# Optimization experiments

Measured on AMD Instinct MI355X. Metric: run time of the kernel, lower is better.

The kernel has to match this reference:

```python
import jax, jax.numpy as jnp
import numpy as np

N_HEAD = 16
D_MODEL = 1024
D_HEAD = D_MODEL // N_HEAD
B, T = 2, 2048


def setup_inputs() -> dict:
    key = jax.random.key(0)
    k1, k2, k3 = jax.random.split(key, 3)
    x = jax.random.normal(k1, (B, T, D_MODEL), dtype=jnp.float32)
    w_attn = jax.random.normal(k2, (3 * D_MODEL, D_MODEL), dtype=jnp.float32) * (D_MODEL ** -0.5)
    w_proj = jax.random.normal(k3, (D_MODEL, D_MODEL), dtype=jnp.float32) * (D_MODEL ** -0.5)
    return {"x": x, "w_attn": w_attn, "w_proj": w_proj}


def _rms_norm(x):
    eps = jnp.asarray(jnp.finfo(x.dtype).eps, x.dtype)
    var = jnp.mean(jnp.square(x), axis=-1, keepdims=True)
    return x * jax.lax.rsqrt(var + eps)


def _rotate_half(x):
    x1, x2 = jnp.split(x, 2, axis=-1)
    return jnp.concatenate((-x2, x1), axis=-1)


def reference(x, w_attn, w_proj):
    Bx, Tx, C = x.shape
    qkv = jnp.einsum('btc,fc->btf', x, w_attn)  # [B,T,3C]
    q, k, v = jnp.split(qkv, 3, axis=-1)
    # [B, H, T, Dh]
    q = q.reshape(Bx, Tx, N_HEAD, D_HEAD).transpose(0, 2, 1, 3)
    k = k.reshape(Bx, Tx, N_HEAD, D_HEAD).transpose(0, 2, 1, 3)
    v = v.reshape(Bx, Tx, N_HEAD, D_HEAD).transpose(0, 2, 1, 3)
    # QK RMSNorm (no learned weight)
    q = _rms_norm(q)
    k = _rms_norm(k)
    # Rotary embedding over full d_head: freqs tiled twice
    inv_freq = 1.0 / (10000.0 ** (jnp.arange(0, D_HEAD, 2, dtype=jnp.float32) / D_HEAD))
    t = jnp.arange(Tx, dtype=jnp.float32)
    freqs = jnp.einsum('i,j->ij', t, inv_freq)  # [T, Dh/2]
    emb = jnp.concatenate((freqs, freqs), axis=-1)  # [T, Dh]
    cos = jnp.cos(emb)[None, None, :, :]
    sin = jnp.sin(emb)[None, None, :, :]
    q = q * cos + _rotate_half(q) * sin
    k = k * cos + _rotate_half(k) * sin
    # Causal SDPA
    scale = D_HEAD ** -0.5
    scores = jnp.einsum('bhqd,bhkd->bhqk', q, k) * scale
    causal = jnp.tril(jnp.ones((Tx, Tx), dtype=bool))
    scores = jnp.where(causal[None, None], scores, jnp.asarray(-jnp.inf, scores.dtype))
    attn = jax.nn.softmax(scores, axis=-1)
    y = jnp.einsum('bhqk,bhkd->bhqd', attn, v)
    y = y.transpose(0, 2, 1, 3).reshape(Bx, Tx, C)
    return jnp.einsum('btc,oc->bto', y, w_proj)
```

## Files before the change

kernel.cpp:

```cpp
#include <hip/hip_runtime.h>
#include <cstdint>
#include <cstddef>


typedef short bf16x8 __attribute__((ext_vector_type(8)));
typedef float floatx4 __attribute__((ext_vector_type(4)));
typedef float floatx2 __attribute__((ext_vector_type(2)));
typedef unsigned short ushortx8 __attribute__((ext_vector_type(8)));
typedef unsigned short ushortx4 __attribute__((ext_vector_type(4)));
typedef unsigned int uintx2 __attribute__((ext_vector_type(2)));

#define DEVI __device__ __forceinline__

DEVI float bf2f(unsigned short u) {
    unsigned int x = ((unsigned int)u) << 16;
    return __builtin_bit_cast(float, x);
}
DEVI unsigned short f2bf(float f) {
    unsigned int u = __builtin_bit_cast(unsigned int, f);
    u += 0x7fffu + ((u >> 16) & 1u);
    return (unsigned short)(u >> 16);
}
DEVI unsigned int pkbf2(float a, float b) {
    unsigned int ua = __builtin_bit_cast(unsigned int, a) + 0x8000u;
    unsigned int ub = __builtin_bit_cast(unsigned int, b) + 0x8000u;
    return __builtin_amdgcn_perm(ub, ua, 0x07060302);
}

DEVI void glds16(const unsigned short* g, unsigned short* l) {
    __builtin_amdgcn_global_load_lds(
        (const __attribute__((address_space(1))) unsigned int*)g,
        (__attribute__((address_space(3))) unsigned int*)l, 16, 0, 0);
}

DEVI void cast8(unsigned short* dst, const float* src) {
    floatx4 a = *(const floatx4*)src;
    floatx4 b = *(const floatx4*)(src + 4);
    ushortx8 o;
    o[0] = f2bf(a[0]); o[1] = f2bf(a[1]); o[2] = f2bf(a[2]); o[3] = f2bf(a[3]);
    o[4] = f2bf(b[0]); o[5] = f2bf(b[1]); o[6] = f2bf(b[2]); o[7] = f2bf(b[3]);
    *(ushortx8*)dst = o;
}

__global__ __launch_bounds__(256)
void cast_inputs(const float* __restrict__ x, const float* __restrict__ wa,
                 const float* __restrict__ wp,
                 unsigned short* __restrict__ xb, unsigned short* __restrict__ wab,
                 unsigned short* __restrict__ wpb, float* __restrict__ ropetab)
{
    size_t g = (size_t)blockIdx.x * 256 + threadIdx.x;
    size_t stride = (size_t)gridDim.x * 256;
    for (size_t i = g; i < (4194304 / 8); i += stride) cast8(xb  + i * 8, x  + i * 8);
    for (size_t i = g; i < (3145728 / 8); i += stride) cast8(wab + i * 8, wa + i * 8);
    for (size_t i = g; i < (1048576 / 8); i += stride) cast8(wpb + i * 8, wp + i * 8);
    for (size_t i = g; i < 65536; i += stride) {
        int t = (int)(i >> 5), f = (int)(i & 31);
        float ang = (float)t * __expf(-(float)f * 0.28782313662425572f);
        float sn, cs;
        __sincosf(ang, &sn, &cs);
        ropetab[2 * i]     = cs;
        ropetab[2 * i + 1] = sn;
    }
}

__global__ __launch_bounds__(512, 2)
void gemm_qkv_8ph(const unsigned short* __restrict__ A,
                  const unsigned short* __restrict__ B,
                  const float* __restrict__ ropetab,
                  unsigned short* __restrict__ Cqk,
                  unsigned short* __restrict__ Vt)
{
    __shared__ __align__(16) unsigned short lds[2][2][256 * 64];

    const int tid  = threadIdx.x;
    const int lane = tid & 63;
    const int w    = tid >> 6;
    const int wm   = w >> 2;
    const int wn   = w & 3;
    const int quad = lane >> 4;
    const int lm   = lane & 15;

    const int lin = blockIdx.y * 12 + blockIdx.x;
    const int s   = (lin & 7) * 24 + (lin >> 3);
    const int m0  = (s / 12) * 256;
    const int n0  = (s % 12) * 256;

    const int srow = tid >> 3;
    const int scol = (((tid & 7) ^ ((tid >> 3) & 7)) * 8);
    const int ldst = w * 512;

#define STG_A(u, WBi, kq) glds16(&A[(size_t)(m0 + (u) * 64 + srow) * 1024 + (kq) + scol], \
                                 &lds[WBi][0][(u) * 4096 + ldst])
#define STG_B(u, WBi, kq) glds16(&B[(size_t)(n0 + (u) * 64 + srow) * 1024 + (kq) + scol], \
                                 &lds[WBi][1][(u) * 4096 + ldst])
#define RD_A(RBi, rrow, kk) (*(const bf16x8*)&lds[RBi][0][(rrow) * 64 + ((((kk) * 4 + quad) ^ ((rrow) & 7)) * 8)])
#define RD_B(RBi, rrow, kk) (*(const bf16x8*)&lds[RBi][1][(rrow) * 64 + ((((kk) * 4 + quad) ^ ((rrow) & 7)) * 8)])

    floatx4 acc[8][4] = {};
    bf16x8 afr[4][2];
    bf16x8 bfr[4][2];

#define MQ(MB, JB)                                                              \
  do {                                                                          \
    _Pragma("unroll")                                                           \
    for (int kk = 0; kk < 2; ++kk)                                              \
      _Pragma("unroll")                                                         \
      for (int mi = 0; mi < 4; ++mi)                                            \
        _Pragma("unroll")                                                       \
        for (int j2 = 0; j2 < 2; ++j2)                                          \
          acc[(MB) + mi][(JB) + j2] = __builtin_amdgcn_mfma_f32_16x16x32_bf16(  \
              afr[mi][kk], bfr[(JB) + j2][kk], acc[(MB) + mi][(JB) + j2], 0, 0, 0); \
  } while (0)

#define TILE(RBi, WBi, KT, LASTF)                                               \
  do {                                                                          \
    const int kn = ((KT) + 1) * 64;                                             \
    if (!(LASTF)) { STG_B(0, WBi, kn); STG_B(1, WBi, kn); }                     \
    _Pragma("unroll")                                                           \
    for (int kk = 0; kk < 2; ++kk) {                                            \
      _Pragma("unroll")                                                         \
      for (int mi = 0; mi < 4; ++mi)                                            \
        afr[mi][kk] = RD_A(RBi, wm * 128 + mi * 16 + lm, kk);                   \
      _Pragma("unroll")                                                         \
      for (int j2 = 0; j2 < 2; ++j2)                                            \
        bfr[j2][kk] = RD_B(RBi, wn * 64 + j2 * 16 + lm, kk);                    \
    }                                                                           \
    asm volatile("s_waitcnt lgkmcnt(8)" ::: "memory");                          \
    __builtin_amdgcn_s_barrier();                                               \
    asm volatile("s_waitcnt lgkmcnt(0)" ::: "memory");                          \
    __builtin_amdgcn_s_setprio(1); MQ(0, 0); __builtin_amdgcn_s_setprio(0);     \
    __builtin_amdgcn_s_barrier();                                               \
    if (!(LASTF)) { STG_B(2, WBi, kn); STG_B(3, WBi, kn); }                     \
    _Pragma("unroll")                                                           \
    for (int kk = 0; kk < 2; ++kk)                                              \
      _Pragma("unroll")                                                         \
      for (int j2 = 0; j2 < 2; ++j2)                                            \
        bfr[2 + j2][kk] = RD_B(RBi, wn * 64 + (2 + j2) * 16 + lm, kk);          \
    if (!(LASTF)) { asm volatile("s_waitcnt vmcnt(4)" ::: "memory"); }          \
    else          { asm volatile("s_waitcnt vmcnt(0)" ::: "memory"); }          \
    __builtin_amdgcn_s_barrier();                                               \
    asm volatile("s_waitcnt lgkmcnt(0)" ::: "memory");                          \
    __builtin_amdgcn_s_setprio(1); MQ(0, 2); __builtin_amdgcn_s_setprio(0);     \
    __builtin_amdgcn_s_barrier();                                               \
    if (!(LASTF)) { STG_A(0, WBi, kn); STG_A(2, WBi, kn); }                     \
    _Pragma("unroll")                                                           \
    for (int kk = 0; kk < 2; ++kk)                                              \
      _Pragma("unroll")                                                         \
      for (int mi = 0; mi < 4; ++mi)                                            \
        afr[mi][kk] = RD_A(RBi, wm * 128 + 64 + mi * 16 + lm, kk);              \
    __builtin_amdgcn_s_barrier();                                               \
    asm volatile("s_waitcnt lgkmcnt(0)" ::: "memory");                          \
    __builtin_amdgcn_s_setprio(1); MQ(4, 2); __builtin_amdgcn_s_setprio(0);     \
    __builtin_amdgcn_s_barrier();                                               \
    if (!(LASTF)) { STG_A(1, WBi, kn); STG_A(3, WBi, kn);                       \
                    asm volatile("s_waitcnt vmcnt(2)" ::: "memory"); }          \
    __builtin_amdgcn_s_barrier();                                               \
    __builtin_amdgcn_s_setprio(1); MQ(4, 0); __builtin_amdgcn_s_setprio(0);     \
    __builtin_amdgcn_s_barrier();                                               \
  } while (0)

    STG_B(0, 0, 0); STG_B(1, 0, 0); STG_B(2, 0, 0); STG_B(3, 0, 0);
    STG_A(0, 0, 0); STG_A(2, 0, 0); STG_A(1, 0, 0); STG_A(3, 0, 0);
    asm volatile("s_waitcnt vmcnt(2)" ::: "memory");
    __builtin_amdgcn_s_barrier();

    for (int kt = 0; kt < 14; kt += 2) {
        TILE(0, 1, kt, false);
        TILE(1, 0, kt + 1, false);
    }
    TILE(0, 1, 14, false);
    TILE(1, 0, 15, true);

    const bool is_v = (n0 + wn * 64) >= 2048;
    if (!is_v) {
        const floatx2* rtab = (const floatx2*)ropetab;
        #pragma unroll
        for (int mi = 0; mi < 8; ++mi) {
            float rn[4];
            #pragma unroll
            for (int r = 0; r < 4; ++r) {
                float ss = 0.0f;
                #pragma unroll
                for (int j = 0; j < 4; ++j) ss += acc[mi][j][r] * acc[mi][j][r];
                ss += __shfl_xor(ss, 1, 64);
                ss += __shfl_xor(ss, 2, 64);
                ss += __shfl_xor(ss, 4, 64);
                ss += __shfl_xor(ss, 8, 64);
                rn[r] = rsqrtf(ss * (1.0f / 64.0f) + 1.1920929e-07f);
            }
            #pragma unroll
            for (int r = 0; r < 4; ++r) {
                int row = m0 + wm * 128 + mi * 16 + quad * 4 + r;
                int t = row & 2047;
                floatx2 cs0 = rtab[t * 32 + lm];
                floatx2 cs1 = rtab[t * 32 + 16 + lm];
                float g = rn[r];
                #pragma unroll
                for (int j = 0; j < 4; ++j) {
                    int d = j * 16 + lm;
                    float cs = (j & 1) ? cs1[0] : cs0[0];
                    float sn = (j & 1) ? cs1[1] : cs0[1];
                    float v  = acc[mi][j][r] * g;
                    float vp = acc[mi][j ^ 2][r] * g;
                    float sgn = (d < 32) ? -1.0f : 1.0f;
                    Cqk[(size_t)row * 2048 + (n0 + wn * 64 + d)] =
                        f2bf(v * cs + sgn * vp * sn);
                }
            }
        }
    } else {
        #pragma unroll
        for (int mi = 0; mi < 8; ++mi)
            #pragma unroll
            for (int j = 0; j < 4; ++j) {
                int col  = n0 + wn * 64 + j * 16 + lm;
                int row0 = m0 + wm * 128 + mi * 16 + quad * 4;
                int bq = row0 >> 11, t0 = row0 & 2047;
                ushortx4 pk;
                #pragma unroll
                for (int r = 0; r < 4; ++r) pk[r] = f2bf(acc[mi][j][r]);
                *(ushortx4*)&Vt[((size_t)(bq * 1024 + (col - 2048))) * 2048 + t0] = pk;
            }
    }
#undef TILE
#undef MQ
#undef RD_A
#undef RD_B
#undef STG_A
#undef STG_B
}

template <int BN, int BK>
__global__ __launch_bounds__(256)
void gemm_bt(const unsigned short* __restrict__ A, const unsigned short* __restrict__ B,
             float* __restrict__ Cf, int M, int N, int K)
{
    constexpr int WCOLS = (BN == 128) ? 2 : 1;
    constexpr int WROWS = 4 / WCOLS;
    constexpr int MI    = 128 / (16 * WROWS);
    constexpr int LPR   = BK / 8;
    constexpr int RPI   = 64 / LPR;

    __shared__ __align__(16) unsigned short As[128 * BK];
    __shared__ __align__(16) unsigned short Bs[BN * BK];

    const int tid  = threadIdx.x;
    const int lane = tid & 63;
    const int w    = tid >> 6;
    const int wm   = w / WCOLS, wn = w % WCOLS;
    const int quad = lane >> 4;
    const int lm   = lane & 15;
    const int m0 = blockIdx.y * 128;
    const int n0 = blockIdx.x * BN;
    const int sr = lane / LPR;
    const int sc = (lane % LPR) * 8;

    floatx4 acc[MI][4] = {};

    for (int k0 = 0; k0 < K; k0 += BK) {
        __syncthreads();
        #pragma unroll
        for (int i = 0; i < 32 / RPI; ++i) {
            int r = w * 32 + i * RPI;
            glds16(&A[(size_t)(m0 + r + sr) * K + k0 + sc], &As[r * BK]);
        }
        #pragma unroll
        for (int i = 0; i < (BN / 4) / RPI; ++i) {
            int r = w * (BN / 4) + i * RPI;
            glds16(&B[(size_t)(n0 + r + sr) * K + k0 + sc], &Bs[r * BK]);
        }
        __syncthreads();

        #pragma unroll
        for (int kk = 0; kk < BK / 32; ++kk) {
            bf16x8 a[MI];
            #pragma unroll
            for (int i = 0; i < MI; ++i)
                a[i] = *(const bf16x8*)&As[(wm * (16 * MI) + i * 16 + lm) * BK + kk * 32 + quad * 8];
            #pragma unroll
            for (int j = 0; j < 4; ++j) {
                bf16x8 b = *(const bf16x8*)&Bs[(wn * 64 + j * 16 + lm) * BK + kk * 32 + quad * 8];
                #pragma unroll
                for (int i = 0; i < MI; ++i)
                    acc[i][j] = __builtin_amdgcn_mfma_f32_16x16x32_bf16(a[i], b, acc[i][j], 0, 0, 0);
            }
        }
    }

    #pragma unroll
    for (int i = 0; i < MI; ++i)
        #pragma unroll
        for (int j = 0; j < 4; ++j) {
            int col  = n0 + wn * 64 + j * 16 + lm;
            int row0 = m0 + wm * (16 * MI) + i * 16 + quad * 4;
            #pragma unroll
            for (int r = 0; r < 4; ++r)
                Cf[(size_t)(row0 + r) * N + col] = acc[i][j][r];
        }
}

#define ATTN_EXP(SA, QROW, PROW, KT, DG)                                       \
  do {                                                                         \
    _Pragma("unroll")                                                          \
    for (int j = 0; j < 4; ++j) {                                              \
      float p0 = exp2f((SA)[j][0] * c1 - c2);                                  \
      float p1 = exp2f((SA)[j][1] * c1 - c2);                                  \
      float p2 = exp2f((SA)[j][2] * c1 - c2);                                  \
      float p3 = exp2f((SA)[j][3] * c1 - c2);                                  \
      if (DG) {                                                                \
        int kb = (KT) * 64 + j * 16 + quad * 4;                                \
        if (kb + 0 > (QROW)) p0 = 0.0f;                                        \
        if (kb + 1 > (QROW)) p1 = 0.0f;                                        \
        if (kb + 2 > (QROW)) p2 = 0.0f;                                        \
        if (kb + 3 > (QROW)) p3 = 0.0f;                                        \
      }                                                                        \
      uintx2 pk;                                                               \
      pk[0] = pkbf2(p0, p1);                                                   \
      pk[1] = pkbf2(p2, p3);                                                   \
      *(uintx2*)&QPs[(PROW) * 64 + (((2 * j + (quad >> 1)) ^ sx) * 8) + (quad & 1) * 4] = pk; \
    }                                                                          \
  } while (0)

#define ATTN_STEP(KSc, VSc, KSn, VSn, KT, DG, LAST)                            \
  do {                                                                         \
    if (!(LAST)) {                                                             \
      *(ushortx8*)&(KSn)[wkA] = kregA; *(ushortx8*)&(KSn)[wkB] = kregB;        \
      *(ushortx8*)&(VSn)[wkA] = vregA; *(ushortx8*)&(VSn)[wkB] = vregB;        \
      if ((KT) + 2 <= lastk) {                                                 \
        kregA = *(const ushortx8*)kpA; kregB = *(const ushortx8*)kpB;          \
        vregA = *(const ushortx8*)vpA; vregB = *(const ushortx8*)vpB;          \
        kpA += (size_t)64 * 2048; kpB += (size_t)64 * 2048;                    \
        vpA += 64; vpB += 64;                                                  \
      }                                                                        \
    }                                                                          \
    floatx4 sa0[4] = {}, sa1[4] = {};                                          \
    _Pragma("unroll")                                                          \
    for (int kk = 0; kk < 2; ++kk)                                             \
      _Pragma("unroll")                                                        \
      for (int j = 0; j < 4; ++j) {                                            \
        bf16x8 kf = *(const bf16x8*)&(KSc)[(j * 16 + lm) * 64 + (((kk * 4 + quad) ^ sx) * 8)]; \
        sa0[j] = __builtin_amdgcn_mfma_f32_16x16x32_bf16(kf, qf0[kk], sa0[j], 0, 0, 0); \
        sa1[j] = __builtin_amdgcn_mfma_f32_16x16x32_bf16(kf, qf1[kk], sa1[j], 0, 0, 0); \
      }                                                                        \
    ATTN_EXP(sa0, qrow0, w * 32 + lm,      KT, DG);                            \
    ATTN_EXP(sa1, qrow1, w * 32 + 16 + lm, KT, DG);                            \
    _Pragma("unroll")                                                          \
    for (int kk = 0; kk < 2; ++kk) {                                           \
      bf16x8 pf0 = *(const bf16x8*)&QPs[(w * 32 + lm) * 64 + (((kk * 4 + quad) ^ sx) * 8)]; \
      bf16x8 pf1 = *(const bf16x8*)&QPs[(w * 32 + 16 + lm) * 64 + (((kk * 4 + quad) ^ sx) * 8)]; \
      _Pragma("unroll")                                                        \
      for (int j = 0; j < 4; ++j) {                                            \
        bf16x8 vf = *(const bf16x8*)&(VSc)[(j * 16 + lm) * 64 + (((kk * 4 + quad) ^ sx) * 8)]; \
        o0[j] = __builtin_amdgcn_mfma_f32_16x16x32_bf16(pf0, vf, o0[j], 0, 0, 0); \
        o1[j] = __builtin_amdgcn_mfma_f32_16x16x32_bf16(pf1, vf, o1[j], 0, 0, 0); \
      }                                                                        \
      l0 = __builtin_amdgcn_mfma_f32_16x16x32_bf16(pf0, ones, l0, 0, 0, 0);    \
      l1 = __builtin_amdgcn_mfma_f32_16x16x32_bf16(pf1, ones, l1, 0, 0, 0);    \
    }                                                                          \
    if (!(LAST)) __syncthreads();                                              \
  } while (0)

__global__ __launch_bounds__(256, 3)
void attention(const unsigned short* __restrict__ qk,
               const unsigned short* __restrict__ Vt,
               unsigned short* __restrict__ Y)
{
    __shared__ __align__(16) unsigned short QPs[128 * 64];
    __shared__ __align__(16) unsigned short Ks0[64 * 64];
    __shared__ __align__(16) unsigned short Ks1[64 * 64];
    __shared__ __align__(16) unsigned short Vs0[64 * 64];
    __shared__ __align__(16) unsigned short Vs1[64 * 64];

    const int tid  = threadIdx.x;
    const int lane = tid & 63;
    const int w    = tid >> 6;
    const int quad = lane >> 4;
    const int lm   = lane & 15;
    const int sx   = lm & 7;

    const int bh = blockIdx.x;
    const int qt = 15 - blockIdx.y;
    const int b  = bh >> 4, h = bh & 15;
    const int q0 = qt * 128;
    const int qrow0 = q0 + w * 32 + lm;
    const int qrow1 = qrow0 + 16;
    const int lastk = 2 * qt + 1;

    const int sr  = tid >> 3;
    const int sch = tid & 7;
    const int swz = ((sch ^ (sr & 7)) * 8);
    const int wkA = sr * 64 + swz;
    const int wkB = (sr + 32) * 64 + swz;

    const unsigned short* kpA = qk + (size_t)b * 2048 * 2048 + 1024 + h * 64
                              + (size_t)sr * 2048 + sch * 8;
    const unsigned short* kpB = kpA + (size_t)32 * 2048;
    const unsigned short* vpA = Vt + (size_t)bh * 64 * 2048 + (size_t)sr * 2048 + sch * 8;
    const unsigned short* vpB = vpA + (size_t)32 * 2048;

    #pragma unroll
    for (int p = 0; p < 4; ++p) {
        int row = p * 32 + sr;
        *(ushortx8*)&QPs[row * 64 + swz] =
            *(const ushortx8*)&qk[((size_t)(b * 2048 + q0 + row)) * 2048 + h * 64 + sch * 8];
    }

    ushortx8 kregA = *(const ushortx8*)kpA, kregB = *(const ushortx8*)kpB;
    ushortx8 vregA = *(const ushortx8*)vpA, vregB = *(const ushortx8*)vpB;
    kpA += (size_t)64 * 2048; kpB += (size_t)64 * 2048; vpA += 64; vpB += 64;
    *(ushortx8*)&Ks0[wkA] = kregA; *(ushortx8*)&Ks0[wkB] = kregB;
    *(ushortx8*)&Vs0[wkA] = vregA; *(ushortx8*)&Vs0[wkB] = vregB;
    kregA = *(const ushortx8*)kpA; kregB = *(const ushortx8*)kpB;
    vregA = *(const ushortx8*)vpA; vregB = *(const ushortx8*)vpB;
    kpA += (size_t)64 * 2048; kpB += (size_t)64 * 2048; vpA += 64; vpB += 64;
    __syncthreads();

    bf16x8 qf0[2], qf1[2];
    #pragma unroll
    for (int kk = 0; kk < 2; ++kk) {
        qf0[kk] = *(const bf16x8*)&QPs[(w * 32 + lm) * 64 + (((kk * 4 + quad) ^ sx) * 8)];
        qf1[kk] = *(const bf16x8*)&QPs[(w * 32 + 16 + lm) * 64 + (((kk * 4 + quad) ^ sx) * 8)];
    }

    bf16x8 ones;
    #pragma unroll
    for (int i = 0; i < 8; ++i) ones[i] = (short)0x3F80;

    floatx4 o0[4] = {}, o1[4] = {};
    floatx4 l0 = {}, l1 = {};
    const float c1 = 0.125f * 1.44269504f;
    const float c2 = 8.0f   * 1.44269504f;

    int kt = 0;
    for (; kt + 3 < 2 * qt + 2; kt += 2) {
        ATTN_STEP(Ks0, Vs0, Ks1, Vs1, kt,     false, false);
        ATTN_STEP(Ks1, Vs1, Ks0, Vs0, kt + 1, false, false);
    }
    ATTN_STEP(Ks0, Vs0, Ks1, Vs1, kt,     true, false);
    ATTN_STEP(Ks1, Vs1, Ks0, Vs0, kt + 1, true, true);

    float rinv0[4], rinv1[4];
    #pragma unroll
    for (int r = 0; r < 4; ++r) { rinv0[r] = 1.0f / l0[r]; rinv1[r] = 1.0f / l1[r]; }

    #pragma unroll
    for (int j = 0; j < 4; ++j) {
        int colg = h * 64 + j * 16 + lm;
        #pragma unroll
        for (int r = 0; r < 4; ++r) {
            int rowg0 = q0 + w * 32 + quad * 4 + r;
            Y[((size_t)(b * 2048 + rowg0)) * 1024 + colg] = f2bf(o0[j][r] * rinv0[r]);
            Y[((size_t)(b * 2048 + rowg0 + 16)) * 1024 + colg] = f2bf(o1[j][r] * rinv1[r]);
        }
    }
}

extern "C" void kernel_launch(void* const* d_in, const int* in_sizes, int n_in,
                              void* d_out, int out_size, void* d_ws, size_t ws_size,
                              hipStream_t stream)
{
    const float* x      = (const float*)d_in[0];
    const float* w_attn = (const float*)d_in[1];
    const float* w_proj = (const float*)d_in[2];
    float* out = (float*)d_out;

    unsigned short* qkbuf = (unsigned short*)d_ws;
    unsigned short* Vtb   = qkbuf + (size_t)4096 * 2048;
    unsigned short* y     = Vtb   + (size_t)32 * 64 * 2048;
    unsigned short* wpb   = y     + (size_t)4096 * 1024;
    unsigned short* xb  = (unsigned short*)d_out;
    unsigned short* wab = xb + (size_t)4096 * 1024;
    float* ropetab = (float*)(wab + (size_t)3072 * 1024);

    dim3 blk(256);
    cast_inputs<<<dim3(1024), blk, 0, stream>>>(x, w_attn, w_proj, xb, wab, wpb, ropetab);
    gemm_qkv_8ph<<<dim3(12, 16), dim3(512), 0, stream>>>(xb, wab, ropetab, qkbuf, Vtb);
    attention<<<dim3(32, 16), dim3(256), 0, stream>>>(qkbuf, Vtb, y);
    gemm_bt<64, 64>
        <<<dim3(16, 32), blk, 0, stream>>>(y, wpb, out, 4096, 1024, 1024);
}
```

Before: 185.8 us.

## Split long causal attention query tiles into two KV halves with reduce pass

Query tiles 8-15, which carry the most causal key blocks, are split into two work items over disjoint key ranges, so every block handles at most 16 key tiles and the grid grows from 16 to 24 items per head. The items run longest-first from a constant table. Split tiles write unnormalised fp32 partial outputs and row sums to scratch (reusing the output buffer), and a new reduce kernel adds the halves, normalises and writes bf16. The aim is better load balance and less tail imbalance, at the cost of an extra launch and fp32 partial traffic. The shared fixed max offset makes the partials directly additive.

```diff
diff --git a/kernel.cpp b/kernel.cpp
--- a/kernel.cpp
+++ b/kernel.cpp
@@ -298,6 +298,16 @@
                 Cf[(size_t)(row0 + r) * N + col] = acc[i][j][r];
         }
 }
+
+#define ENC(qt, t0, nt) ((qt) | ((t0) << 8) | ((nt) << 16))
+__constant__ int g_items[24] = {
+    ENC(15,16,16), ENC(15,0,16), ENC(14,0,16), ENC(13,0,16), ENC(12,0,16),
+    ENC(11,0,16),  ENC(10,0,16), ENC(9,0,16),  ENC(8,0,16),  ENC(7,0,16),
+    ENC(14,16,14), ENC(6,0,14),  ENC(13,16,12), ENC(5,0,12),
+    ENC(12,16,10), ENC(4,0,10),  ENC(11,16,8),  ENC(3,0,8),
+    ENC(10,16,6),  ENC(2,0,6),   ENC(9,16,4),   ENC(1,0,4),
+    ENC(8,16,2),   ENC(0,0,2)
+};
 
 #define ATTN_EXP(SA, QROW, PROW, KT, DG)                                       \
   do {                                                                         \
@@ -363,7 +373,8 @@
 __global__ __launch_bounds__(256, 3)
 void attention(const unsigned short* __restrict__ qk,
                const unsigned short* __restrict__ Vt,
-               unsigned short* __restrict__ Y)
+               unsigned short* __restrict__ Y,
+               float* __restrict__ Po, float* __restrict__ Pl)
 {
     __shared__ __align__(16) unsigned short QPs[128 * 64];
     __shared__ __align__(16) unsigned short Ks0[64 * 64];
@@ -379,12 +390,17 @@
     const int sx   = lm & 7;
 
     const int bh = blockIdx.x;
-    const int qt = 15 - blockIdx.y;
+    const int it = g_items[blockIdx.y];
+    const int qt = it & 255;
+    const int t0 = (it >> 8) & 255;
+    const int nt = it >> 16;
     const int b  = bh >> 4, h = bh & 15;
     const int q0 = qt * 128;
     const int qrow0 = q0 + w * 32 + lm;
     const int qrow1 = qrow0 + 16;
-    const int lastk = 2 * qt + 1;
+    const int lastk = t0 + nt - 1;
+    const bool mflag = (t0 + nt) == (2 * qt + 2);
+    const bool partial = qt >= 8;
 
     const int sr  = tid >> 3;
     const int sch = tid & 7;
@@ -393,9 +409,10 @@
     const int wkB = (sr + 32) * 64 + swz;
 
     const unsigned short* kpA = qk + (size_t)b * 2048 * 2048 + 1024 + h * 64
-                              + (size_t)sr * 2048 + sch * 8;
+                              + (size_t)(t0 * 64 + sr) * 2048 + sch * 8;
     const unsigned short* kpB = kpA + (size_t)32 * 2048;
-    const unsigned short* vpA = Vt + (size_t)bh * 64 * 2048 + (size_t)sr * 2048 + sch * 8;
+    const unsigned short* vpA = Vt + (size_t)bh * 64 * 2048 + (size_t)sr * 2048
+                              + t0 * 64 + sch * 8;
     const unsigned short* vpB = vpA + (size_t)32 * 2048;
 
     #pragma unroll
@@ -431,27 +448,81 @@
     const float c1 = 0.125f * 1.44269504f;
     const float c2 = 8.0f   * 1.44269504f;
 
-    int kt = 0;
-    for (; kt + 3 < 2 * qt + 2; kt += 2) {
-        ATTN_STEP(Ks0, Vs0, Ks1, Vs1, kt,     false, false);
-        ATTN_STEP(Ks1, Vs1, Ks0, Vs0, kt + 1, false, false);
-    }
-    ATTN_STEP(Ks0, Vs0, Ks1, Vs1, kt,     true, false);
-    ATTN_STEP(Ks1, Vs1, Ks0, Vs0, kt + 1, true, true);
-
-    float rinv0[4], rinv1[4];
+    int ct = 0;
+    for (; ct + 3 < nt; ct += 2) {
+        ATTN_STEP(Ks0, Vs0, Ks1, Vs1, t0 + ct,     false, false);
+        ATTN_STEP(Ks1, Vs1, Ks0, Vs0, t0 + ct + 1, false, false);
+    }
+    ATTN_STEP(Ks0, Vs0, Ks1, Vs1, t0 + ct,     mflag, false);
+    ATTN_STEP(Ks1, Vs1, Ks0, Vs0, t0 + ct + 1, mflag, true);
+
+    if (!partial) {
+        float rinv0[4], rinv1[4];
+        #pragma unroll
+        for (int r = 0; r < 4; ++r) { rinv0[r] = 1.0f / l0[r]; rinv1[r] = 1.0f / l1[r]; }
+        #pragma unroll
+        for (int j = 0; j < 4; ++j) {
+            int colg = h * 64 + j * 16 + lm;
+            #pragma unroll
+            for (int r = 0; r < 4; ++r) {
+                int rowg0 = q0 + w * 32 + quad * 4 + r;
+                Y[((size_t)(b * 2048 + rowg0)) * 1024 + colg] = f2bf(o0[j][r] * rinv0[r]);
+                Y[((size_t)(b * 2048 + rowg0 + 16)) * 1024 + colg] = f2bf(o1[j][r] * rinv1[r]);
+            }
+        }
+    } else {
+        const int pidx = (bh * 8 + (qt - 8)) * 2 + (t0 ? 1 : 0);
+        float* po = Po + (size_t)pidx * 8192;
+        #pragma unroll
+        for (int j = 0; j < 4; ++j)
+            #pragma unroll
+            for (int r = 0; r < 4; ++r) {
+                int row0 = w * 32 + quad * 4 + r;
+                po[row0 * 64 + j * 16 + lm]        = o0[j][r];
+                po[(row0 + 16) * 64 + j * 16 + lm] = o1[j][r];
+            }
+        if (lm == 0) {
+            float* pl = Pl + (size_t)pidx * 128;
+            #pragma unroll
+            for (int r = 0; r < 4; ++r) {
+                pl[w * 32 + quad * 4 + r]      = l0[r];
+                pl[w * 32 + 16 + quad * 4 + r] = l1[r];
+            }
+        }
+    }
+}
+
+__global__ __launch_bounds__(256)
+void attn_reduce(const float* __restrict__ Po, const float* __restrict__ Pl,
+                 unsigned short* __restrict__ Y)
+{
+    const int bh = blockIdx.x, qi = blockIdx.y;
+    const int b = bh >> 4, h = bh & 15;
+    const int q0 = (8 + qi) * 128;
+    const int tid = threadIdx.x;
+    const int row = tid >> 1;
+    const int c0  = (tid & 1) * 32;
+    const size_t base = ((size_t)(bh * 8 + qi)) * 2;
+    const float* po0 = Po + (base + 0) * 8192 + row * 64 + c0;
+    const float* po1 = Po + (base + 1) * 8192 + row * 64 + c0;
+    const float rinv = 1.0f / (Pl[(base + 0) * 128 + row] + Pl[(base + 1) * 128 + row]);
+    unsigned short* yp = Y + ((size_t)(b * 2048 + q0 + row)) * 1024 + h * 64 + c0;
     #pragma unroll
-    for (int r = 0; r < 4; ++r) { rinv0[r] = 1.0f / l0[r]; rinv1[r] = 1.0f / l1[r]; }
-
-    #pragma unroll
-    for (int j = 0; j < 4; ++j) {
-        int colg = h * 64 + j * 16 + lm;
-        #pragma unroll
-        for (int r = 0; r < 4; ++r) {
-            int rowg0 = q0 + w * 32 + quad * 4 + r;
-            Y[((size_t)(b * 2048 + rowg0)) * 1024 + colg] = f2bf(o0[j][r] * rinv0[r]);
-            Y[((size_t)(b * 2048 + rowg0 + 16)) * 1024 + colg] = f2bf(o1[j][r] * rinv1[r]);
-        }
+    for (int c = 0; c < 4; ++c) {
+        floatx4 a  = *(const floatx4*)(po0 + c * 8);
+        floatx4 a2 = *(const floatx4*)(po0 + c * 8 + 4);
+        floatx4 e  = *(const floatx4*)(po1 + c * 8);
+        floatx4 e2 = *(const floatx4*)(po1 + c * 8 + 4);
+        ushortx8 o;
+        o[0] = f2bf((a[0]  + e[0])  * rinv);
+        o[1] = f2bf((a[1]  + e[1])  * rinv);
+        o[2] = f2bf((a[2]  + e[2])  * rinv);
+        o[3] = f2bf((a[3]  + e[3])  * rinv);
+        o[4] = f2bf((a2[0] + e2[0]) * rinv);
+        o[5] = f2bf((a2[1] + e2[1]) * rinv);
+        o[6] = f2bf((a2[2] + e2[2]) * rinv);
+        o[7] = f2bf((a2[3] + e2[3]) * rinv);
+        *(ushortx8*)(yp + c * 8) = o;
     }
 }
 
@@ -468,14 +539,17 @@
     unsigned short* Vtb   = qkbuf + (size_t)4096 * 2048;
     unsigned short* y     = Vtb   + (size_t)32 * 64 * 2048;
     unsigned short* wpb   = y     + (size_t)4096 * 1024;
+    float* Plb            = (float*)(wpb + (size_t)1024 * 1024);
     unsigned short* xb  = (unsigned short*)d_out;
     unsigned short* wab = xb + (size_t)4096 * 1024;
     float* ropetab = (float*)(wab + (size_t)3072 * 1024);
+    float* Pob = (float*)d_out;
 
     dim3 blk(256);
     cast_inputs<<<dim3(1024), blk, 0, stream>>>(x, w_attn, w_proj, xb, wab, wpb, ropetab);
     gemm_qkv_8ph<<<dim3(12, 16), dim3(512), 0, stream>>>(xb, wab, ropetab, qkbuf, Vtb);
-    attention<<<dim3(32, 16), dim3(256), 0, stream>>>(qkbuf, Vtb, y);
+    attention<<<dim3(32, 24), blk, 0, stream>>>(qkbuf, Vtb, y, Pob, Plb);
+    attn_reduce<<<dim3(32, 8), blk, 0, stream>>>(Pob, Plb, y);
     gemm_bt<64, 64>
         <<<dim3(16, 32), blk, 0, stream>>>(y, wpb, out, 4096, 1024, 1024);
 }
```

Result: faster. 181.0 us (-2.6%).
